# Kernel tuning notes

Measured on AMD Instinct MI355X. Metric: run time of the kernel, lower is better.

Reference implementation:

```python
import jax, jax.numpy as jnp
import numpy as np

N = 6            # wall nodes of a shoebox room
NM1 = N - 1
NL = N * NM1     # 30 node-to-node delay lines
FIR = 7          # fir_order
SR = 16000
C = 343.0
G = C / SR       # meters per sample
ALPHA = 0.02
ROOM = np.array([4.0, 3.0, 2.5])
B, T = 4, 4000
# incoming line i is fed by outgoing line PERM[i]  (torch: permutation_matrix @ v)
PERM = np.array([(6 * (i + 1) - i % N - 1) % NL for i in range(NL)], dtype=np.int32)
PAIRS = [(i, m) for i in range(N) for m in range(N) if m != i]


def _geometry(src, mic):
    # SDN first-order reflection nodes: image source projected through each wall
    Bm = mic.shape[0]
    nodes = np.zeros((Bm, N, 3))
    j = 0
    for a in range(3):
        for w in (0.0, float(ROOM[a])):
            img = src.copy()
            img[a] = 2.0 * w - src[a]
            t = (w - img[a]) / (mic[:, a] - img[a])          # (B,)
            nodes[:, j] = img[None, :] + t[:, None] * (mic - img[None, :])
            j += 1
    d_sn = np.linalg.norm(nodes - src[None, None, :], axis=2)   # (B,N)
    d_nm = np.linalg.norm(nodes - mic[:, None, :], axis=2)      # (B,N)
    d_sm = np.linalg.norm(mic - src[None, :], axis=1)           # (B,)
    d_nn = np.stack([np.linalg.norm(nodes[:, i] - nodes[:, m], axis=1) for i, m in PAIRS], axis=1)  # (B,NL)
    return d_sn, d_nn, d_nm, d_sm


def _run(x, junction_filters, junction_vs, pressure_weights, src_np, mic_np):
    d_sn, d_nn, d_nm, d_sm = _geometry(src_np, mic_np)
    Bc = mic_np.shape[0]
    src_g = jnp.asarray(0.5 * G / d_sn, jnp.float32)            # source_gains (B,N)
    mic_g = jnp.asarray(1.0 / (1.0 + d_nm / d_sn), jnp.float32)  # mic_gains (B,N)
    dir_g = jnp.asarray(1.0 / d_sm, jnp.float32)                # (B,)
    D_sn = np.rint(d_sn / G).astype(np.int32)
    D_nn = np.rint(d_nn / G).astype(np.int32)
    D_nm = np.rint(d_nm / G).astype(np.int32)
    D_sm = np.rint(d_sm / G).astype(np.int32)
    L1 = int(D_sn.max()) + 1
    L2 = int(D_nn.max()) + 1 + FIR
    L3 = int(D_nm.max()) + 1 + FIR
    L4 = int(D_sm.max()) + 1
    d_sn_j = jnp.asarray(D_sn)
    d_nn_j = jnp.asarray(D_nn)
    d_nm_j = jnp.asarray(D_nm)
    d_sm_j = jnp.asarray(D_sm)
    taps = jnp.arange(FIR + 1, dtype=jnp.int32)   # extra delay per reversed coeff
    filt_rev = junction_filters[:, ::-1]          # last torch coeff acts at nominal delay
    filt_rev_lines = jnp.repeat(filt_rev, NM1, axis=0)           # (NL,FIR+1)
    uu = jnp.sum(junction_vs * junction_vs, axis=1)              # (N,)
    eye = jnp.eye(NM1, dtype=junction_vs.dtype)
    S = 2.0 * jnp.einsum('ni,nj->nij', junction_vs, junction_vs) / uu[:, None, None] - eye[None]
    perm = jnp.asarray(PERM)
    pw3 = pressure_weights.reshape(N, NM1)

    def step(carry, inp):
        pp, b1, b2, b3, b4 = carry
        xk, k = inp
        # source -> nodes (plain integer delay line, write then read)
        b1 = b1.at[:, :, k % L1].set(src_g * xk)
        inj = jnp.take_along_axis(b1, ((k - d_sn_j) % L1)[:, :, None], axis=2)[..., 0]
        pp = pp + jnp.repeat(inj, NM1, axis=1)                   # (B,NL)
        # Householder scattering at each junction (block-diagonal over nodes)
        pm = jnp.einsum('nij,bnj->bni', S, pp.reshape(Bc, N, NM1)).reshape(Bc, NL)
        # node pressures -> mic (FIR-filtered delay)
        pnode = jnp.einsum('bnj,nj->bn', pm.reshape(Bc, N, NM1), pw3)
        b3 = b3.at[:, :, k % L3].set(mic_g * pnode)
        idx3 = (k - d_nm_j[:, :, None] - taps) % L3              # (B,N,FIR+1)
        ym = jnp.einsum('bnj,nj->bn', jnp.take_along_axis(b3, idx3, axis=2), filt_rev).sum(1)
        # direct source -> mic path (plain delay)
        b4 = b4.at[:, 0, k % L4].set(xk)
        yd = dir_g * jnp.take_along_axis(b4, ((k - d_sm_j) % L4)[:, None, None], axis=2)[:, 0, 0]
        # nodes -> nodes (FIR-filtered delay lines) then permutation
        b2 = b2.at[:, :, k % L2].set(pm)
        idx2 = (k - d_nn_j[:, :, None] - taps) % L2              # (B,NL,FIR+1)
        delayed = jnp.einsum('blj,lj->bl', jnp.take_along_axis(b2, idx2, axis=2), filt_rev_lines)
        pp_next = delayed[:, perm]
        return (pp_next, b1, b2, b3, b4), ym + yd

    carry0 = (jnp.zeros((Bc, NL), jnp.float32),
              jnp.zeros((Bc, N, L1), jnp.float32),
              jnp.zeros((Bc, NL, L2), jnp.float32),
              jnp.zeros((Bc, N, L3), jnp.float32),
              jnp.zeros((Bc, 1, L4), jnp.float32))
    ks = jnp.arange(x.shape[0], dtype=jnp.int32)
    _, ys = jax.lax.scan(step, carry0, (x, ks))
    return ys.T   # (B,T)


def setup_inputs():
    key = jax.random.key(0)
    k = jax.random.split(key, 6)
    x = jax.random.normal(k[0], (T,), dtype=jnp.float32)
    room = jnp.asarray(ROOM, jnp.float32)
    src_pos = room * (0.25 + 0.5 * jax.random.uniform(k[1], (3,), dtype=jnp.float32))
    mic_pos = room * (0.25 + 0.5 * jax.random.uniform(k[2], (B, 3), dtype=jnp.float32))
    beta = float(np.sqrt(1.0 - ALPHA))
    junction_filters = (jnp.zeros((N, FIR + 1), jnp.float32).at[:, -1].set(beta)
                        + 0.01 * jax.random.normal(k[3], (N, FIR + 1), dtype=jnp.float32))
    junction_vs = jnp.ones((N, NM1), jnp.float32) + 0.05 * jax.random.normal(k[4], (N, NM1), dtype=jnp.float32)
    pressure_weights = ((2.0 / NM1) * jnp.ones((NL,), jnp.float32)
                        + 0.01 * jax.random.normal(k[5], (NL,), dtype=jnp.float32))
    return {"x": x, "src_pos": src_pos, "mic_pos": mic_pos,
            "junction_filters": junction_filters, "junction_vs": junction_vs,
            "pressure_weights": pressure_weights}


def reference(x, src_pos, mic_pos, junction_filters, junction_vs, pressure_weights):
    src_np = np.asarray(src_pos, np.float64)
    mic_np = np.asarray(mic_pos, np.float64)
    return _run(x, junction_filters, junction_vs, pressure_weights, src_np, mic_np)
```

## Files before the change

### kernel.cpp

```cpp
#include <hip/hip_runtime.h>
#include <math.h>


#define NN    6
#define NLn   30
#define FIRN  7
#define TLEN  4000
#define LCAP  448
#define EXT   13
#define HEAD  32
#define RSTRA (LCAP + EXT + HEAD)
#define PADX  264
#define XPAD  64
#define NROW  37
#define BATCH 56
#define SPW   7
#define NU    (SPW + FIRN)

template<int CTRL>
__device__ __forceinline__ float dpp_add(float x) {
    int m = __builtin_amdgcn_update_dpp(0, __float_as_int(x), CTRL, 0xF, 0xF, false);
    return x + __int_as_float(m);
}
__device__ __forceinline__ float dpp_xquad(float x) {
    int xi = __float_as_int(x);
    int m = __builtin_amdgcn_update_dpp(0, xi, 0x114, 0xF, 0xA, false);
    m     = __builtin_amdgcn_update_dpp(m, xi, 0x104, 0xF, 0x5, false);
    return __int_as_float(m);
}

__global__ __launch_bounds__(512)
void sdn_kernel(const float* __restrict__ x, const float* __restrict__ srcp,
                const float* __restrict__ micp, const float* __restrict__ jf,
                const float* __restrict__ jv, const float* __restrict__ pw,
                float* __restrict__ out, int T)
{
    const int b   = blockIdx.x;
    const int l   = threadIdx.x;
    const int wl  = l & 63;
    const int wid = l >> 6;

    __shared__ float  rows[NROW][RSTRA];
    __shared__ float  xl[PADX + TLEN + XPAD];
    __shared__ float  st[NN + 1][BATCH + 1];
    __shared__ double nds[NN][3];
    __shared__ int    sshift[NROW];

    for (int i = l; i < NROW * RSTRA;       i += 512) (&rows[0][0])[i] = 0.f;
    for (int i = l; i < PADX + TLEN + XPAD; i += 512) xl[i] = 0.f;
    __syncthreads();
    for (int i = l; i < T; i += 512) xl[PADX + i] = x[i];

    const double room[3] = {4.0, 3.0, 2.5};
    double src[3] = {srcp[0], srcp[1], srcp[2]};
    double mic[3] = {micp[3*b+0], micp[3*b+1], micp[3*b+2]};

    if (l < NN) {
        int a = l >> 1;
        double w = (l & 1) ? room[a] : 0.0;
        double sa = (a == 0) ? src[0] : ((a == 1) ? src[1] : src[2]);
        double ma = (a == 0) ? mic[0] : ((a == 1) ? mic[1] : mic[2]);
        double ia = 2.0 * w - sa;
        double img0 = src[0], img1 = src[1], img2 = src[2];
        if (a == 0) img0 = ia; else if (a == 1) img1 = ia; else img2 = ia;
        double t = (w - ia) / (ma - ia);
        nds[l][0] = img0 + t * (mic[0] - img0);
        nds[l][1] = img1 + t * (mic[1] - img1);
        nds[l][2] = img2 + t * (mic[2] - img2);
    }
    __syncthreads();

    const double G = 343.0 / 16000.0;
    const int n  = (wl < 48) ? (wl >> 3) : 0;
    const int ir = wl & 7;
    const bool isline = (wl < 48) && (ir < 5);
    const bool ismic  = (wl < 48) && (ir == 5);
    const bool isdir  = (wl == 6);

    const int lineid = n * 5 + ir;
    #define PERMF(i) ((6*((i)+1) - ((i)%6) - 1) % NLn)
    const int srcl = PERMF(lineid % NLn);
    #undef PERMF
    const int ns = srcl / 5;

    double dx = nds[n][0] - src[0], dy = nds[n][1] - src[1], dz = nds[n][2] - src[2];
    double dsn = sqrt(dx*dx + dy*dy + dz*dz);
    dx = nds[n][0] - mic[0]; dy = nds[n][1] - mic[1]; dz = nds[n][2] - mic[2];
    double dnm = sqrt(dx*dx + dy*dy + dz*dz);
    dx = mic[0] - src[0]; dy = mic[1] - src[1]; dz = mic[2] - src[2];
    double dsm = sqrt(dx*dx + dy*dy + dz*dz);

    const int   Dsn  = (int)rint(dsn / G);
    const int   Dsm  = (int)rint(dsm / G);
    const float srcg = (float)(0.5 * G / dsn);
    const float micg = (float)(1.0 / (1.0 + dnm / dsn));
    const float dirg = (float)(1.0 / dsm);

    int Dline;
    {
        int mm = srcl % 5;
        int m2 = mm + (mm >= ns ? 1 : 0);
        double ax = nds[ns][0] - nds[m2][0];
        double ay = nds[ns][1] - nds[m2][1];
        double az = nds[ns][2] - nds[m2][2];
        Dline = (int)rint(sqrt(ax*ax + ay*ay + az*az) / G);
    }
    const int Dmic = (int)rint(dnm / G);
    const int D = isline ? Dline : (ismic ? Dmic : 64);

    float srcgl; int xoff;
    if (isline)      { srcgl = srcg; xoff = PADX - Dsn; }
    else if (isdir)  { srcgl = dirg; xoff = PADX - Dsm - BATCH; }
    else             { srcgl = 0.f;  xoff = PADX; }

    const int nc = isline ? ns : n;
    const bool hasfir = isline || ismic;
    float c0,c1,c2,c3,c4,c5,c6,c7;
    {
        const float* f = jf + nc*(FIRN+1);
        c0 = hasfir ? f[7] : 0.f; c1 = hasfir ? f[6] : 0.f;
        c2 = hasfir ? f[5] : 0.f; c3 = hasfir ? f[4] : 0.f;
        c4 = hasfir ? f[3] : 0.f; c5 = hasfir ? f[2] : 0.f;
        c6 = hasfir ? f[1] : 0.f; c7 = hasfir ? f[0] : 0.f;
    }

    const float uu = jv[n*5+0]*jv[n*5+0] + jv[n*5+1]*jv[n*5+1] + jv[n*5+2]*jv[n*5+2]
                   + jv[n*5+3]*jv[n*5+3] + jv[n*5+4]*jv[n*5+4];
    const float c2u = 2.0f / uu;
    const float vw = isline ? jv[n*5+ir] : 0.f;
    const float qw = isline ? micg * pw[n*5+ir] : 0.f;
    float Wa;
    if (isline) Wa = vw;
    else if (ismic) {
        Wa = micg * (jv[n*5+0]*pw[n*5+0] + jv[n*5+1]*pw[n*5+1] + jv[n*5+2]*pw[n*5+2]
                   + jv[n*5+3]*pw[n*5+3] + jv[n*5+4]*pw[n*5+4]);
    } else Wa = 0.f;

    const int rdrow = isline ? srcl : (ismic ? NLn + n : NROW - 1);
    const int wrrow = isline ? lineid : (ismic ? NLn + n : NROW - 1);
    const bool haswrite = isline || ismic;
    const bool hasstage = ismic || isdir;

    const int k0off = SPW * wid;
    const int shift = isline ? 8 : 7;
    const int lag   = isline ? 0 : BATCH;

    if (wid == 0) {
        if (isline || ismic) {
            int v = ((wl & 31) - rdrow * RSTRA + shift + D + lag) % 32;
            sshift[rdrow] = (v + 32) % 32;
        }
        if (l == 0) {
            int v = (6 - (NROW-1) * RSTRA + 7 + 64 + BATCH) % 32;
            sshift[NROW-1] = (v + 32) % 32;
        }
    }
    __syncthreads();

    float* rdbase = &rows[rdrow][0] + sshift[rdrow];
    float* wrbase = &rows[wrrow][0] + sshift[wrrow];
    float* strow  = st[ismic ? n : 6];
    const float* xpc = xl + xoff;
    float* outp = out + b * T;

    int cur_off = ((k0off - shift - D - lag) % LCAP + LCAP) % LCAP;
    int wp0 = 0;
    const int NB = (T + BATCH - 1) / BATCH;

    float u[NU], xq[SPW];
    #pragma unroll
    for (int j = 0; j < NU; ++j) u[j] = rdbase[cur_off + j];
    #pragma unroll
    for (int i = 0; i < SPW; ++i) xq[i] = xpc[k0off + i];
    cur_off += BATCH; if (cur_off >= LCAP) cur_off -= LCAP;

    for (int m = 0; m <= NB; ++m) {
        float fir[SPW], inj[SPW], p[SPW];
        #pragma unroll
        for (int i = 0; i < SPW; ++i) {
            float a = c7 * u[i];
            a = fmaf(c6, u[i+1], a); a = fmaf(c5, u[i+2], a);
            a = fmaf(c4, u[i+3], a); a = fmaf(c3, u[i+4], a);
            a = fmaf(c2, u[i+5], a); a = fmaf(c1, u[i+6], a);
            a = fmaf(c0, u[i+7], a);
            inj[i] = srcgl * xq[i];
            if (isdir) a = inj[i];
            fir[i] = a;
            p[i] = a + inj[i];
        }

        float wv[SPW];
        #pragma unroll
        for (int i = 0; i < SPW; ++i) {
            float tv = vw * p[i];
            float tq = qw * p[i];
            tv = dpp_add<0xB1>(tv); tq = dpp_add<0xB1>(tq);
            tv = dpp_add<0x4E>(tv); tq = dpp_add<0x4E>(tq);
            float Av = tv + dpp_xquad(tv);
            float Bv = tq + dpp_xquad(tq);
            float s  = Av * c2u;
            wv[i] = fmaf(s, Wa, -(ismic ? Bv : p[i]));
        }

        if (haswrite) {
            #pragma unroll
            for (int i = 0; i < SPW; ++i) wrbase[wp0 + k0off + i] = wv[i];
        }
        if (wp0 == 0) {
            if (haswrite) {
                #pragma unroll
                for (int i = 0; i < SPW; ++i)
                    if (k0off + i < EXT) wrbase[LCAP + k0off + i] = wv[i];
            }
        }
        if (hasstage) {
            #pragma unroll
            for (int i = 0; i < SPW; ++i) strow[k0off + i] = fir[i];
        }

        __syncthreads();

        if (m < NB) {
            #pragma unroll
            for (int j = 0; j < NU; ++j) u[j] = rdbase[cur_off + j];
            #pragma unroll
            for (int i = 0; i < SPW; ++i) xq[i] = xpc[(m+1)*BATCH + k0off + i];
            cur_off += BATCH; if (cur_off >= LCAP) cur_off -= LCAP;
        }

        if (wl < SPW) {
            int col  = k0off + wl;
            int gidx = (m - 1) * BATCH + col;
            if ((unsigned)gidx < (unsigned)T) {
                float ssum = ((st[0][col] + st[1][col]) + (st[2][col] + st[3][col]))
                           + ((st[4][col] + st[5][col]) + st[6][col]);
                outp[gidx] = ssum;
            }
        }

        wp0 += BATCH; if (wp0 >= LCAP) wp0 -= LCAP;
    }
}

extern "C" void kernel_launch(void* const* d_in, const int* in_sizes, int n_in,
                              void* d_out, int out_size, void* d_ws, size_t ws_size,
                              hipStream_t stream)
{
    const float* x    = (const float*)d_in[0];
    const float* srcp = (const float*)d_in[1];
    const float* micp = (const float*)d_in[2];
    const float* jf   = (const float*)d_in[3];
    const float* jv   = (const float*)d_in[4];
    const float* pw   = (const float*)d_in[5];
    float* out = (float*)d_out;

    int T  = in_sizes[0];
    if (T > TLEN) T = TLEN;
    int Bc = in_sizes[2] / 3;

    sdn_kernel<<<Bc, 512, 0, stream>>>(x, srcp, micp, jf, jv, pw, out, T);
}
```

Measured before the change: 86.56 us.

## Move mic/direct output reduction into idle lanes with DPP row sums

Mic FIR outputs and the direct path move from lanes in each node group to a separate lane group (48-54), and the output sum is taken with DPP row-shift adds instead of staging to shared memory and summing in a few lanes. This removes the shared staging array, its writes and reads, and the serialized 7-row sum per batch. The cost is extra lanes doing FIR work and seven DPP reductions per batch run by every lane. Lane 55 writes the result, relying on a prefix-sum pattern that must give the full sum of lanes 48-55.

Result: slower. 97.73 us (+12.9%).

```diff
diff --git a/kernel.cpp b/kernel.cpp
--- a/kernel.cpp
+++ b/kernel.cpp
@@ -28,6 +28,12 @@
     m     = __builtin_amdgcn_update_dpp(m, xi, 0x104, 0xF, 0x5, false);
     return __int_as_float(m);
 }
+__device__ __forceinline__ float dpp_sum8(float x) {
+    x = dpp_add<0x111>(x);
+    x = dpp_add<0x112>(x);
+    x = dpp_add<0x114>(x);
+    return x;
+}
 
 __global__ __launch_bounds__(512)
 void sdn_kernel(const float* __restrict__ x, const float* __restrict__ srcp,
@@ -42,7 +48,6 @@
 
     __shared__ float  rows[NROW][RSTRA];
     __shared__ float  xl[PADX + TLEN + XPAD];
-    __shared__ float  st[NN + 1][BATCH + 1];
     __shared__ double nds[NN][3];
     __shared__ int    sshift[NROW];
 
@@ -71,11 +76,12 @@
     __syncthreads();
 
     const double G = 343.0 / 16000.0;
-    const int n  = (wl < 48) ? (wl >> 3) : 0;
     const int ir = wl & 7;
     const bool isline = (wl < 48) && (ir < 5);
     const bool ismic  = (wl < 48) && (ir == 5);
-    const bool isdir  = (wl == 6);
+    const bool ismicf = (wl >= 48) && (wl < 54);
+    const bool isdir  = (wl == 54);
+    const int n = (wl < 48) ? (wl >> 3) : (ismicf ? (wl - 48) : 0);
 
     const int lineid = n * 5 + ir;
     #define PERMF(i) ((6*((i)+1) - ((i)%6) - 1) % NLn)
@@ -106,7 +112,7 @@
         Dline = (int)rint(sqrt(ax*ax + ay*ay + az*az) / G);
     }
     const int Dmic = (int)rint(dnm / G);
-    const int D = isline ? Dline : (ismic ? Dmic : 64);
+    const int D = isline ? Dline : (ismicf ? Dmic : 64);
 
     float srcgl; int xoff;
     if (isline)      { srcgl = srcg; xoff = PADX - Dsn; }
@@ -114,7 +120,7 @@
     else             { srcgl = 0.f;  xoff = PADX; }
 
     const int nc = isline ? ns : n;
-    const bool hasfir = isline || ismic;
+    const bool hasfir = isline || ismicf;
     float c0,c1,c2,c3,c4,c5,c6,c7;
     {
         const float* f = jf + nc*(FIRN+1);
@@ -136,17 +142,17 @@
                    + jv[n*5+3]*pw[n*5+3] + jv[n*5+4]*pw[n*5+4]);
     } else Wa = 0.f;
 
-    const int rdrow = isline ? srcl : (ismic ? NLn + n : NROW - 1);
+    const int rdrow = isline ? srcl : (ismicf ? NLn + n : NROW - 1);
     const int wrrow = isline ? lineid : (ismic ? NLn + n : NROW - 1);
     const bool haswrite = isline || ismic;
-    const bool hasstage = ismic || isdir;
+    const bool hasout   = (wl >= 48) && (wl <= 54);
 
     const int k0off = SPW * wid;
     const int shift = isline ? 8 : 7;
     const int lag   = isline ? 0 : BATCH;
 
     if (wid == 0) {
-        if (isline || ismic) {
+        if (isline || ismicf) {
             int v = ((wl & 31) - rdrow * RSTRA + shift + D + lag) % 32;
             sshift[rdrow] = (v + 32) % 32;
         }
@@ -159,7 +165,6 @@
 
     float* rdbase = &rows[rdrow][0] + sshift[rdrow];
     float* wrbase = &rows[wrrow][0] + sshift[wrrow];
-    float* strow  = st[ismic ? n : 6];
     const float* xpc = xl + xoff;
     float* outp = out + b * T;
 
@@ -213,10 +218,6 @@
                     if (k0off + i < EXT) wrbase[LCAP + k0off + i] = wv[i];
             }
         }
-        if (hasstage) {
-            #pragma unroll
-            for (int i = 0; i < SPW; ++i) strow[k0off + i] = fir[i];
-        }
 
         __syncthreads();
 
@@ -228,14 +229,12 @@
             cur_off += BATCH; if (cur_off >= LCAP) cur_off -= LCAP;
         }
 
-        if (wl < SPW) {
-            int col  = k0off + wl;
-            int gidx = (m - 1) * BATCH + col;
-            if ((unsigned)gidx < (unsigned)T) {
-                float ssum = ((st[0][col] + st[1][col]) + (st[2][col] + st[3][col]))
-                           + ((st[4][col] + st[5][col]) + st[6][col]);
-                outp[gidx] = ssum;
-            }
+        #pragma unroll
+        for (int i = 0; i < SPW; ++i) {
+            float z = hasout ? fir[i] : 0.f;
+            z = dpp_sum8(z);
+            int gidx = (m - 1) * BATCH + k0off + i;
+            if (wl == 55 && (unsigned)gidx < (unsigned)T) outp[gidx] = z;
         }
 
         wp0 += BATCH; if (wp0 >= LCAP) wp0 -= LCAP;
```
